# Kernel optimization log

Measured on AMD Instinct MI355X. Metric: run time of the kernel, lower is better.

## Reference

```python
import jax, jax.numpy as jnp
import numpy as np

EPS = 1e-6
DIAG_SIZE = 128  # triu band half-width (init kwarg diag_size)
NEG_INF = -1e9


def feature_map(x):
    # tanh feature map: phi(x) = tanh(x) + 1 (positive feature map)
    return jnp.tanh(x) + 1.0


def causal_dot_product(Q, K, V):
    # Q,K: [N,L,H,E], V: [N,L,H,D]
    # running KV state: S_l = sum_{s<=l} K_s V_s^T, materialized via cumsum
    kv = jnp.cumsum(jnp.einsum('nlhe,nlhd->nlhed', K, V), axis=1)  # [N,L,H,E,D]
    return jnp.einsum('nlhe,nlhed->nlhd', Q, kv)


def setup_inputs() -> dict:
    key = jax.random.key(0)
    k1, k2, k3 = jax.random.split(key, 3)
    N, L, H, E = 2, 2048, 8, 64
    queries = jax.random.normal(k1, (N, L, H, E), dtype=jnp.float32)
    keys = jax.random.normal(k2, (N, L, H, E), dtype=jnp.float32)
    values = jax.random.normal(k3, (N, L, H, E), dtype=jnp.float32)
    key_lengths_mask = jnp.ones((N, L), dtype=jnp.float32)  # all keys valid
    blend = jnp.full((1,), 0.9, dtype=jnp.float32)  # learned blend param (init 0.9)
    return {"queries": queries, "keys": keys, "values": values,
            "key_lengths_mask": key_lengths_mask, "blend": blend}


def reference(queries, keys, values, key_lengths_mask, blend):
    N, L, H, E = queries.shape
    # ---- linear attention path (kernel_1 = tanh, kernel_2 = 'none') ----
    Q1 = feature_map(queries)
    K1 = feature_map(keys) * key_lengths_mask[:, :, None, None]
    Z1 = 1.0 / (jnp.einsum('nlhi,nlhi->nlh', Q1, jnp.cumsum(K1, axis=1)) + EPS)
    LV = causal_dot_product(Q1, K1, values) * Z1[..., None]  # [N,L,H,D]
    # ---- full softmax attention path (banded by triu) ----
    softmax_temp = 1.0 / np.sqrt(E).astype(np.float32)
    QK = jnp.einsum('nlhe,nshe->nhls', queries, keys)  # [N,H,L,L]
    l_idx = jnp.arange(L)[:, None]
    s_idx = jnp.arange(L)[None, :]
    causal_add = jnp.where(s_idx <= l_idx, 0.0, NEG_INF)  # lower-triangular mask
    key_add = jnp.where(key_lengths_mask > 0, 0.0, NEG_INF)  # [N,L]
    logits = softmax_temp * (QK + causal_add[None, None] + key_add[:, None, None, :])
    A = jax.nn.softmax(logits, axis=-1)
    # torch.triu(A, diagonal=-diag_size): keep s >= l - diag_size
    band = s_idx >= (l_idx - DIAG_SIZE)
    A = jnp.where(band[None, None], A, 0.0)
    # dropout: eval mode (identity)
    SV = jnp.einsum('nhls,nshd->nlhd', A, values)
    b = blend[0]
    return b * SV + (1.0 - b) * LV
```

## Files before the change

### kernel.cpp

```cpp
#include <hip/hip_runtime.h>
#include <math.h>

#define N_ 2
#define L_ 2048
#define H_ 8
#define E_ 64
#define D_ 64
#define C_ 128
#define NC (L_/C_)
#define ROWSTRIDE (H_*E_)
#define TEMP 0.125f
#define EPS_F 1e-6f
#define NEG_INF_F (-1e9f)
#define CHUNK_WS (E_*D_ + E_)
#define NCHUNKS (N_*H_*NC)
#define TPAD 136
#define PPAD 72

typedef __attribute__((ext_vector_type(8))) short short8;
typedef __attribute__((ext_vector_type(4))) float f32x4;

__device__ __forceinline__ short f2bf(float x) {
  unsigned u = __float_as_uint(x);
  u += 0x7fffu + ((u >> 16) & 1u);
  return (short)(u >> 16);
}
__device__ __forceinline__ float bf2f(short s) {
  return __uint_as_float(((unsigned)(unsigned short)s) << 16);
}
__device__ __forceinline__ float tanh1f(float x) {
  float e = __expf(-2.f * x);
  return 2.f * __builtin_amdgcn_rcpf(1.f + e);
}

__device__ __forceinline__ void load_bf16_tile(short* __restrict__ dst,
                                               const float* __restrict__ src) {
  const int t = threadIdx.x;
#pragma unroll
  for (int it = 0; it < 4; ++it) {
    int gi = it * 256 + t;
    int row = gi >> 3, g = gi & 7;
    const float* p = src + row * ROWSTRIDE + g * 8;
    float4 a = *(const float4*)p;
    float4 b = *(const float4*)(p + 4);
    short8 v;
    v[0] = f2bf(a.x); v[1] = f2bf(a.y); v[2] = f2bf(a.z); v[3] = f2bf(a.w);
    v[4] = f2bf(b.x); v[5] = f2bf(b.y); v[6] = f2bf(b.z); v[7] = f2bf(b.w);
    int sg = g ^ (row & 7);
    *(short8*)(dst + row * 64 + sg * 8) = v;
  }
}

__device__ __forceinline__ short8 frag_ld(const short* __restrict__ buf,
                                          int rowbase, int hf, int lane) {
  int r = rowbase + (lane & 15);
  int g = (hf * 4 + (lane >> 4)) ^ (r & 7);
  return *(const short8*)(buf + r * 64 + g * 8);
}
__device__ __forceinline__ short8 frag_ldT(const short* __restrict__ buf,
                                           int nbase, int g, int lane) {
  int r = nbase + (lane & 15);
  return *(const short8*)(buf + r * TPAD + g * 8);
}
__device__ __forceinline__ short8 frag_ldP(const short* __restrict__ buf,
                                           int rowbase, int ks, int lane) {
  int r = rowbase + (lane & 15);
  int g = ks * 4 + (lane >> 4);
  return *(const short8*)(buf + r * PPAD + g * 8);
}

extern "C" __global__ void __launch_bounds__(256)
k_pre(const float* __restrict__ Q, const float* __restrict__ K,
      const float* __restrict__ V, const float* __restrict__ mask,
      float* __restrict__ ws, float* __restrict__ part) {
  __shared__ short ldsA[64 * TPAD];
  __shared__ short ldsB[64 * TPAD];
  __shared__ float fmsk[C_];
  const int orig = blockIdx.x;
  const int swz = (orig & 7) * 304 + (orig >> 3);
  const int t = threadIdx.x;
  const int w = t >> 6, lane = t & 63;
  const int col_lo = lane & 15;

  if (swz < 2176) {
    const int nh = swz / 136;
    const int p = swz - nh * 136;
    int qb = (int)((sqrtf(8.f * p + 1.f) - 1.f) * 0.5f);
    while ((qb + 1) * (qb + 2) / 2 <= p) ++qb;
    while (qb * (qb + 1) / 2 > p) --qb;
    const int kb = p - qb * (qb + 1) / 2;
    const int h = nh & (H_ - 1), n = nh >> 3;

    load_bf16_tile(ldsA, Q + ((n * L_ + qb * C_) * H_ + h) * E_);
    load_bf16_tile(ldsB, K + ((n * L_ + kb * C_) * H_ + h) * E_);
    if (t < C_) fmsk[t] = mask[n * L_ + kb * C_ + t];
    __syncthreads();

    const int rowbase = w * 32;
    short8 afr[2][2];
#pragma unroll
    for (int m = 0; m < 2; ++m)
#pragma unroll
      for (int hh = 0; hh < 2; ++hh)
        afr[m][hh] = frag_ld(ldsA, rowbase + 16 * m, hh, lane);

    f32x4 acc[2][8];
#pragma unroll
    for (int m = 0; m < 2; ++m)
#pragma unroll
      for (int c = 0; c < 8; ++c) acc[m][c] = (f32x4){0.f, 0.f, 0.f, 0.f};

#pragma unroll
    for (int c = 0; c < 8; ++c) {
      short8 b0 = frag_ld(ldsB, 16 * c, 0, lane);
      short8 b1 = frag_ld(ldsB, 16 * c, 1, lane);
#pragma unroll
      for (int m = 0; m < 2; ++m) {
        acc[m][c] = __builtin_amdgcn_mfma_f32_16x16x32_bf16(afr[m][0], b0, acc[m][c], 0, 0, 0);
        acc[m][c] = __builtin_amdgcn_mfma_f32_16x16x32_bf16(afr[m][1], b1, acc[m][c], 0, 0, 0);
      }
    }

    const bool diag = (kb == qb);
    float* pout = part + (size_t)(nh * NC + qb) * C_ * 16;
#pragma unroll
    for (int m = 0; m < 2; ++m) {
      const int rbase = rowbase + 16 * m + ((lane >> 4) << 2);
      float rs[4] = {0.f, 0.f, 0.f, 0.f};
#pragma unroll
      for (int c = 0; c < 8; ++c) {
        const int col = 16 * c + col_lo;
        const float madd = (fmsk[col] > 0.f) ? 0.f : NEG_INF_F;
#pragma unroll
        for (int reg = 0; reg < 4; ++reg) {
          float x = acc[m][c][reg] + madd;
          if (diag && col > rbase + reg) x += NEG_INF_F;
          rs[reg] += __expf(x * TEMP);
        }
      }
#pragma unroll
      for (int off = 1; off < 16; off <<= 1) {
#pragma unroll
        for (int reg = 0; reg < 4; ++reg) rs[reg] += __shfl_xor(rs[reg], off);
      }
      if (col_lo == 0) {
#pragma unroll
        for (int reg = 0; reg < 4; ++reg) pout[(rbase + reg) * 16 + kb] = rs[reg];
      }
    }
  } else {
    const int id = swz - 2176;
    const int nh = id >> 4, c = id & 15;
    const int h = nh & (H_ - 1), n = nh >> 3;
    const int gbase = ((n * L_ + c * C_) * H_ + h) * E_;
    const int e = t & 63, sb = t >> 6;
    const int mbase = n * L_ + c * C_;
#pragma unroll
    for (int q = 0; q < 4; ++q) {
      int s0 = sb * 32 + q * 8;
      short8 kk, vv;
#pragma unroll
      for (int j = 0; j < 8; ++j) {
        float kx = K[gbase + (s0 + j) * ROWSTRIDE + e];
        kk[j] = f2bf(tanh1f(kx) * mask[mbase + s0 + j]);
        vv[j] = f2bf(V[gbase + (s0 + j) * ROWSTRIDE + e]);
      }
      *(short8*)(ldsA + e * TPAD + (s0 >> 3) * 8) = kk;
      *(short8*)(ldsB + e * TPAD + (s0 >> 3) * 8) = vv;
    }
    __syncthreads();

    f32x4 acc[4];
#pragma unroll
    for (int nn = 0; nn < 4; ++nn) acc[nn] = (f32x4){0.f, 0.f, 0.f, 0.f};
#pragma unroll
    for (int ks = 0; ks < 4; ++ks) {
      short8 a = frag_ldT(ldsB, 16 * w, ks * 4 + (lane >> 4), lane);
#pragma unroll
      for (int nn = 0; nn < 4; ++nn) {
        short8 b = frag_ldT(ldsA, 16 * nn, ks * 4 + (lane >> 4), lane);
        acc[nn] = __builtin_amdgcn_mfma_f32_16x16x32_bf16(a, b, acc[nn], 0, 0, 0);
      }
    }
    float* wsc = ws + (size_t)(nh * NC + c) * CHUNK_WS;
    const int drow = 16 * w + ((lane >> 4) << 2);
#pragma unroll
    for (int nn = 0; nn < 4; ++nn)
#pragma unroll
      for (int reg = 0; reg < 4; ++reg)
        wsc[(16 * nn + col_lo) * D_ + drow + reg] = acc[nn][reg];
    if (t < 64) {
      float s = 0.f;
#pragma unroll
      for (int g = 0; g < 16; ++g) {
        short8 v = *(const short8*)(ldsA + t * TPAD + g * 8);
#pragma unroll
        for (int j = 0; j < 8; ++j) s += bf2f(v[j]);
      }
      wsc[E_ * D_ + t] = s;
    }
  }
}

extern "C" __global__ void __launch_bounds__(256)
k_scan(float* __restrict__ ws) {
  const int bid = blockIdx.x;
  const int swz = (bid & 7) * 34 + (bid >> 3);
  const int nh = swz / 17, seg = swz - nh * 17;
  const int idx = seg * 256 + threadIdx.x;
  if (idx >= CHUNK_WS) return;
  float* base = ws + (size_t)nh * NC * CHUNK_WS + idx;
  float v[NC];
#pragma unroll
  for (int c = 0; c < NC; ++c) v[c] = base[(size_t)c * CHUNK_WS];
  float acc = 0.f;
#pragma unroll
  for (int c = 0; c < NC; ++c) {
    base[(size_t)c * CHUNK_WS] = acc;
    acc += v[c];
  }
}

extern "C" __global__ void __launch_bounds__(256, 2)
k_fused(const float* __restrict__ Q, const float* __restrict__ K,
        const float* __restrict__ V, const float* __restrict__ mask,
        const float* __restrict__ blend, const float* __restrict__ ws,
        const float* __restrict__ part, float* __restrict__ out) {
  __shared__ short kbuf[C_ * 64];
  __shared__ short kv[64 * TPAD];
  __shared__ short pbuf[64 * PPAD];
  __shared__ float zlds[64];
  __shared__ float dinv[64];
  __shared__ float ksum[E_];
  __shared__ float kmC[C_];
  __shared__ float kmP[C_];

  const int orig = blockIdx.x;
  const int swz = (orig & 7) * 64 + (orig >> 3);
  const int rh = swz & 1, qb = (swz >> 1) & (NC - 1), nh = swz >> 5;
  const int h = nh & (H_ - 1), n = nh >> 3;
  const int t = threadIdx.x;
  const int w = t >> 6, lane = t & 63;
  const int rowbase = w * 16;
  const int col_lo = lane & 15;
  const int rb = rowbase + ((lane >> 4) << 2);
  const int rtile0 = rh * 64 + rb;
  const int qgbase = ((n * L_ + qb * C_ + rh * 64) * H_ + h) * E_;
  const int kbase_chunk = ((n * L_ + qb * C_) * H_ + h) * E_;
  const float* wsc = ws + (size_t)(nh * NC + qb) * CHUNK_WS;
  const float bl = blend[0];
  const float ob = 1.f - bl;
  const int d = t & 63, sb = t >> 6;
  const bool haveprev = (qb > 0);
  const int kgp = ((n * L_ + (qb - 1) * C_) * H_ + h) * E_;

  {
    const float* mrow = mask + n * L_ + qb * C_;
#pragma unroll
    for (int it = 0; it < 4; ++it) {
      int gi = it * 256 + t, row = gi >> 3, g = gi & 7;
      const float* p = K + kbase_chunk + row * ROWSTRIDE + g * 8;
      float4 a = *(const float4*)p, b = *(const float4*)(p + 4);
      float km = mrow[row];
      float xs[8] = {a.x, a.y, a.z, a.w, b.x, b.y, b.z, b.w};
      short8 v1;
#pragma unroll
      for (int j = 0; j < 8; ++j) v1[j] = f2bf(tanh1f(xs[j]) * km);
      *(short8*)(kbuf + row * 64 + (g ^ (row & 7)) * 8) = v1;
    }
  }
  {
    int eb = t >> 6;
#pragma unroll
    for (int q = 0; q < 2; ++q) {
      int e0 = eb * 16 + q * 8;
      short8 v;
#pragma unroll
      for (int j = 0; j < 8; ++j) v[j] = f2bf(wsc[(e0 + j) * D_ + d]);
      *(short8*)(kv + d * TPAD + (e0 >> 3) * 8) = v;
    }
  }
  if (t < 64) {
    ksum[t] = wsc[E_ * D_ + t];
    const float* pb = part + ((size_t)(nh * NC + qb) * C_ + rh * 64 + t) * 16;
    float4 a = *(const float4*)pb, b = *(const float4*)(pb + 4);
    float4 c = *(const float4*)(pb + 8), d4 = *(const float4*)(pb + 12);
    float vv[16] = {a.x, a.y, a.z, a.w, b.x, b.y, b.z, b.w,
                    c.x, c.y, c.z, c.w, d4.x, d4.y, d4.z, d4.w};
    float s = 0.f;
#pragma unroll
    for (int j = 0; j < 16; ++j) s += (j <= qb) ? vv[j] : 0.f;
    dinv[t] = 1.f / s;
  }
  if (t < C_) {
    kmC[t] = mask[n * L_ + qb * C_ + t];
    kmP[t] = haveprev ? mask[n * L_ + (qb - 1) * C_ + t] : 1.f;
  }
  __syncthreads();

  short8 af1[2];
  {
    const float* qp = Q + qgbase + (rowbase + (lane & 15)) * ROWSTRIDE;
#pragma unroll
    for (int kh = 0; kh < 2; ++kh) {
      int c0 = (kh * 4 + (lane >> 4)) * 8;
      float4 a = *(const float4*)(qp + c0);
      float4 b = *(const float4*)(qp + c0 + 4);
      float xs[8] = {a.x, a.y, a.z, a.w, b.x, b.y, b.z, b.w};
#pragma unroll
      for (int j = 0; j < 8; ++j) af1[kh][j] = f2bf(tanh1f(xs[j]));
    }
  }
  f32x4 c1[8];
#pragma unroll
  for (int ct = 0; ct < 8; ++ct) c1[ct] = (f32x4){0.f, 0.f, 0.f, 0.f};
#pragma unroll
  for (int ct = 0; ct < 8; ++ct) {
    short8 b0 = frag_ld(kbuf, 16 * ct, 0, lane);
    short8 b1 = frag_ld(kbuf, 16 * ct, 1, lane);
    c1[ct] = __builtin_amdgcn_mfma_f32_16x16x32_bf16(af1[0], b0, c1[ct], 0, 0, 0);
    c1[ct] = __builtin_amdgcn_mfma_f32_16x16x32_bf16(af1[1], b1, c1[ct], 0, 0, 0);
  }
  {
    float zz = 0.f;
#pragma unroll
    for (int kh = 0; kh < 2; ++kh) {
      int cb = (kh * 4 + (lane >> 4)) * 8;
#pragma unroll
      for (int j = 0; j < 8; ++j) zz += bf2f(af1[kh][j]) * ksum[cb + j];
    }
    zz += __shfl_xor(zz, 16);
    zz += __shfl_xor(zz, 32);
    if (lane < 16) zlds[rowbase + lane] = zz;
  }
  float rs[4] = {0.f, 0.f, 0.f, 0.f};
#pragma unroll
  for (int ct = 0; ct < 8; ++ct) {
    int col = 16 * ct + col_lo;
#pragma unroll
    for (int reg = 0; reg < 4; ++reg) {
      if (col <= rtile0 + reg) rs[reg] += c1[ct][reg];
      else c1[ct][reg] = 0.f;
    }
  }
#pragma unroll
  for (int off = 1; off < 16; off <<= 1)
#pragma unroll
    for (int reg = 0; reg < 4; ++reg) rs[reg] += __shfl_xor(rs[reg], off);

  f32x4 accO[4];
#pragma unroll
  for (int nn = 0; nn < 4; ++nn) accO[nn] = (f32x4){0.f, 0.f, 0.f, 0.f};
#pragma unroll
  for (int ks = 0; ks < 2; ++ks) {
    short8 bf[4];
#pragma unroll
    for (int nn = 0; nn < 4; ++nn)
      bf[nn] = frag_ldT(kv, 16 * nn, ks * 4 + (lane >> 4), lane);
#pragma unroll
    for (int nn = 0; nn < 4; ++nn)
      accO[nn] = __builtin_amdgcn_mfma_f32_16x16x32_bf16(af1[ks], bf[nn], accO[nn], 0, 0, 0);
  }
  float zrf[4], sdv[4];
#pragma unroll
  for (int reg = 0; reg < 4; ++reg) {
    zrf[reg] = ob / (zlds[rb + reg] + rs[reg] + EPS_F);
    sdv[reg] = bl * dinv[rb + reg];
  }
#pragma unroll
  for (int nn = 0; nn < 4; ++nn)
#pragma unroll
    for (int reg = 0; reg < 4; ++reg) accO[nn][reg] *= zrf[reg];
#pragma unroll
  for (int ct = 0; ct < 8; ++ct)
#pragma unroll
    for (int reg = 0; reg < 4; ++reg) c1[ct][reg] *= zrf[reg];
  __syncthreads();

#pragma unroll
  for (int it = 0; it < 4; ++it) {
    int gi = it * 256 + t, row = gi >> 3, g = gi & 7;
    const float* p = K + kbase_chunk + row * ROWSTRIDE + g * 8;
    float4 a = *(const float4*)p, b = *(const float4*)(p + 4);
    short8 v;
    v[0] = f2bf(a.x); v[1] = f2bf(a.y); v[2] = f2bf(a.z); v[3] = f2bf(a.w);
    v[4] = f2bf(b.x); v[5] = f2bf(b.y); v[6] = f2bf(b.z); v[7] = f2bf(b.w);
    *(short8*)(kbuf + row * 64 + (g ^ (row & 7)) * 8) = v;
  }
#pragma unroll
  for (int q = 0; q < 4; ++q) {
    int s0 = sb * 32 + q * 8;
    short8 v;
#pragma unroll
    for (int j = 0; j < 8; ++j) v[j] = f2bf(V[kbase_chunk + (s0 + j) * ROWSTRIDE + d]);
    *(short8*)(kv + d * TPAD + (s0 >> 3) * 8) = v;
  }
  __syncthreads();

#pragma unroll
  for (int hh = 0; hh < 2; ++hh) {
#pragma unroll
    for (int ch = 0; ch < 4; ++ch) {
      int ct = 4 * hh + ch, colh = 16 * ch + col_lo;
#pragma unroll
      for (int reg = 0; reg < 4; ++reg)
        pbuf[(rb + reg) * PPAD + colh] = f2bf(c1[ct][reg]);
    }
#pragma unroll
    for (int ks = 0; ks < 2; ++ks) {
      short8 ap = frag_ldP(pbuf, rowbase, ks, lane);
      short8 bv[4];
#pragma unroll
      for (int nn = 0; nn < 4; ++nn)
        bv[nn] = frag_ldT(kv, 16 * nn, 8 * hh + ks * 4 + (lane >> 4), lane);
#pragma unroll
      for (int nn = 0; nn < 4; ++nn)
        accO[nn] = __builtin_amdgcn_mfma_f32_16x16x32_bf16(ap, bv[nn], accO[nn], 0, 0, 0);
    }
  }

  {
    short8 afs[2];
    const float* qp = Q + qgbase + (rowbase + (lane & 15)) * ROWSTRIDE;
#pragma unroll
    for (int kh = 0; kh < 2; ++kh) {
      int c0 = (kh * 4 + (lane >> 4)) * 8;
      float4 a = *(const float4*)(qp + c0);
      float4 b = *(const float4*)(qp + c0 + 4);
      float xs[8] = {a.x, a.y, a.z, a.w, b.x, b.y, b.z, b.w};
#pragma unroll
      for (int j = 0; j < 8; ++j) afs[kh][j] = f2bf(xs[j]);
    }
#pragma unroll
    for (int ct = 0; ct < 8; ++ct) c1[ct] = (f32x4){0.f, 0.f, 0.f, 0.f};
#pragma unroll
    for (int ct = 0; ct < 8; ++ct) {
      short8 b0 = frag_ld(kbuf, 16 * ct, 0, lane);
      short8 b1 = frag_ld(kbuf, 16 * ct, 1, lane);
      c1[ct] = __builtin_amdgcn_mfma_f32_16x16x32_bf16(afs[0], b0, c1[ct], 0, 0, 0);
      c1[ct] = __builtin_amdgcn_mfma_f32_16x16x32_bf16(afs[1], b1, c1[ct], 0, 0, 0);
    }
#pragma unroll
    for (int ct = 0; ct < 8; ++ct) {
      int col = 16 * ct + col_lo;
      float madd = (kmC[col] > 0.f) ? 0.f : NEG_INF_F;
#pragma unroll
      for (int reg = 0; reg < 4; ++reg) {
        float x = c1[ct][reg] + madd;
        if (col > rtile0 + reg) x += NEG_INF_F;
        c1[ct][reg] = sdv[reg] * __expf(x * TEMP);
      }
    }
#pragma unroll
    for (int hh = 0; hh < 2; ++hh) {
#pragma unroll
      for (int ch = 0; ch < 4; ++ch) {
        int ct = 4 * hh + ch, colh = 16 * ch + col_lo;
#pragma unroll
        for (int reg = 0; reg < 4; ++reg)
          pbuf[(rb + reg) * PPAD + colh] = f2bf(c1[ct][reg]);
      }
#pragma unroll
      for (int ks = 0; ks < 2; ++ks) {
        short8 ap = frag_ldP(pbuf, rowbase, ks, lane);
        short8 bv[4];
#pragma unroll
        for (int nn = 0; nn < 4; ++nn)
          bv[nn] = frag_ldT(kv, 16 * nn, 8 * hh + ks * 4 + (lane >> 4), lane);
#pragma unroll
        for (int nn = 0; nn < 4; ++nn)
          accO[nn] = __builtin_amdgcn_mfma_f32_16x16x32_bf16(ap, bv[nn], accO[nn], 0, 0, 0);
      }
    }
  }

  if (haveprev) {
    __syncthreads();
#pragma unroll
    for (int it = 0; it < 4; ++it) {
      int gi = it * 256 + t, row = gi >> 3, g = gi & 7;
      const float* p = K + kgp + row * ROWSTRIDE + g * 8;
      float4 a = *(const float4*)p, b = *(const float4*)(p + 4);
      short8 v;
      v[0] = f2bf(a.x); v[1] = f2bf(a.y); v[2] = f2bf(a.z); v[3] = f2bf(a.w);
      v[4] = f2bf(b.x); v[5] = f2bf(b.y); v[6] = f2bf(b.z); v[7] = f2bf(b.w);
      *(short8*)(kbuf + row * 64 + (g ^ (row & 7)) * 8) = v;
    }
#pragma unroll
    for (int q = 0; q < 4; ++q) {
      int s0 = sb * 32 + q * 8;
      short8 v;
#pragma unroll
      for (int j = 0; j < 8; ++j) v[j] = f2bf(V[kgp + (s0 + j) * ROWSTRIDE + d]);
      *(short8*)(kv + d * TPAD + (s0 >> 3) * 8) = v;
    }
    __syncthreads();

    short8 afs[2];
    const float* qp = Q + qgbase + (rowbase + (lane & 15)) * ROWSTRIDE;
#pragma unroll
    for (int kh = 0; kh < 2; ++kh) {
      int c0 = (kh * 4 + (lane >> 4)) * 8;
      float4 a = *(const float4*)(qp + c0);
      float4 b = *(const float4*)(qp + c0 + 4);
      float xs[8] = {a.x, a.y, a.z, a.w, b.x, b.y, b.z, b.w};
#pragma unroll
      for (int j = 0; j < 8; ++j) afs[kh][j] = f2bf(xs[j]);
    }
#pragma unroll
    for (int ct = 0; ct < 8; ++ct) c1[ct] = (f32x4){0.f, 0.f, 0.f, 0.f};
#pragma unroll
    for (int ct = 0; ct < 8; ++ct) {
      short8 b0 = frag_ld(kbuf, 16 * ct, 0, lane);
      short8 b1 = frag_ld(kbuf, 16 * ct, 1, lane);
      c1[ct] = __builtin_amdgcn_mfma_f32_16x16x32_bf16(afs[0], b0, c1[ct], 0, 0, 0);
      c1[ct] = __builtin_amdgcn_mfma_f32_16x16x32_bf16(afs[1], b1, c1[ct], 0, 0, 0);
    }
#pragma unroll
    for (int ct = 0; ct < 8; ++ct) {
      int col = 16 * ct + col_lo;
      float madd = (kmP[col] > 0.f) ? 0.f : NEG_INF_F;
#pragma unroll
      for (int reg = 0; reg < 4; ++reg) {
        float x = c1[ct][reg] + madd;
        float pp = sdv[reg] * __expf(x * TEMP);
        if (col < rtile0 + reg) pp = 0.f;
        c1[ct][reg] = pp;
      }
    }
#pragma unroll
    for (int hh = 0; hh < 2; ++hh) {
#pragma unroll
      for (int ch = 0; ch < 4; ++ch) {
        int ct = 4 * hh + ch, colh = 16 * ch + col_lo;
#pragma unroll
        for (int reg = 0; reg < 4; ++reg)
          pbuf[(rb + reg) * PPAD + colh] = f2bf(c1[ct][reg]);
      }
#pragma unroll
      for (int ks = 0; ks < 2; ++ks) {
        short8 ap = frag_ldP(pbuf, rowbase, ks, lane);
        short8 bv[4];
#pragma unroll
        for (int nn = 0; nn < 4; ++nn)
          bv[nn] = frag_ldT(kv, 16 * nn, 8 * hh + ks * 4 + (lane >> 4), lane);
#pragma unroll
        for (int nn = 0; nn < 4; ++nn)
          accO[nn] = __builtin_amdgcn_mfma_f32_16x16x32_bf16(ap, bv[nn], accO[nn], 0, 0, 0);
      }
    }
  }

#pragma unroll
  for (int nn = 0; nn < 4; ++nn)
#pragma unroll
    for (int reg = 0; reg < 4; ++reg)
      out[qgbase + (rb + reg) * ROWSTRIDE + 16 * nn + col_lo] = accO[nn][reg];
}

extern "C" void kernel_launch(void* const* d_in, const int* in_sizes, int n_in,
                              void* d_out, int out_size, void* d_ws, size_t ws_size,
                              hipStream_t stream) {
  (void)in_sizes; (void)n_in; (void)out_size; (void)ws_size;
  const float* Q = (const float*)d_in[0];
  const float* K = (const float*)d_in[1];
  const float* V = (const float*)d_in[2];
  const float* mask = (const float*)d_in[3];
  const float* blend = (const float*)d_in[4];
  float* out = (float*)d_out;
  float* ws = (float*)d_ws;
  float* part = ws + (size_t)NCHUNKS * CHUNK_WS;

  k_pre<<<dim3(2432), dim3(256), 0, stream>>>(Q, K, V, mask, ws, part);
  k_scan<<<dim3(272), dim3(256), 0, stream>>>(ws);
  k_fused<<<dim3(N_ * H_ * NC * 2), dim3(256), 0, stream>>>(Q, K, V, mask, blend, ws, part, out);
}
```

Baseline: 48.17 us.

## Reuse band-tile exp scores from pre-pass instead of recomputing QK in fused kernel

The pre-pass, which already computes QK scores for every causal tile, now also writes unnormalized bf16 exp values for the diagonal and previous-diagonal tiles to workspace. The fused kernel reads these probability tiles directly instead of reloading K, recomputing QK with MFMA and redoing the exp. Row normalisation is applied once at the end through a separate accumulator. This trades recompute for extra global writes and reads, about 2 x 32 KB per chunk, and adds write traffic to the pre-pass.

```diff
diff --git a/kernel.cpp b/kernel.cpp
--- a/kernel.cpp
+++ b/kernel.cpp
@@ -33,8 +33,9 @@
   return 2.f * __builtin_amdgcn_rcpf(1.f + e);
 }
 
-__device__ __forceinline__ void load_bf16_tile(short* __restrict__ dst,
-                                               const float* __restrict__ src) {
+template <typename F>
+__device__ __forceinline__ void stage_tile(short* __restrict__ dst,
+                                           const float* __restrict__ src, F f) {
   const int t = threadIdx.x;
 #pragma unroll
   for (int it = 0; it < 4; ++it) {
@@ -43,11 +44,11 @@
     const float* p = src + row * ROWSTRIDE + g * 8;
     float4 a = *(const float4*)p;
     float4 b = *(const float4*)(p + 4);
+    float xs[8] = {a.x, a.y, a.z, a.w, b.x, b.y, b.z, b.w};
     short8 v;
-    v[0] = f2bf(a.x); v[1] = f2bf(a.y); v[2] = f2bf(a.z); v[3] = f2bf(a.w);
-    v[4] = f2bf(b.x); v[5] = f2bf(b.y); v[6] = f2bf(b.z); v[7] = f2bf(b.w);
-    int sg = g ^ (row & 7);
-    *(short8*)(dst + row * 64 + sg * 8) = v;
+#pragma unroll
+    for (int j = 0; j < 8; ++j) v[j] = f2bf(f(xs[j], row));
+    *(short8*)(dst + row * 64 + (g ^ (row & 7)) * 8) = v;
   }
 }
 
@@ -72,7 +73,8 @@
 extern "C" __global__ void __launch_bounds__(256)
 k_pre(const float* __restrict__ Q, const float* __restrict__ K,
       const float* __restrict__ V, const float* __restrict__ mask,
-      float* __restrict__ ws, float* __restrict__ part) {
+      float* __restrict__ ws, float* __restrict__ part,
+      short* __restrict__ pd, short* __restrict__ pp) {
   __shared__ short ldsA[64 * TPAD];
   __shared__ short ldsB[64 * TPAD];
   __shared__ float fmsk[C_];
@@ -91,8 +93,10 @@
     const int kb = p - qb * (qb + 1) / 2;
     const int h = nh & (H_ - 1), n = nh >> 3;
 
-    load_bf16_tile(ldsA, Q + ((n * L_ + qb * C_) * H_ + h) * E_);
-    load_bf16_tile(ldsB, K + ((n * L_ + kb * C_) * H_ + h) * E_);
+    stage_tile(ldsA, Q + ((n * L_ + qb * C_) * H_ + h) * E_,
+               [](float x, int) { return x; });
+    stage_tile(ldsB, K + ((n * L_ + kb * C_) * H_ + h) * E_,
+               [](float x, int) { return x; });
     if (t < C_) fmsk[t] = mask[n * L_ + kb * C_ + t];
     __syncthreads();
 
@@ -122,6 +126,9 @@
     }
 
     const bool diag = (kb == qb);
+    const bool prev = (kb == qb - 1);
+    const bool band = diag || prev;
+    short* pt = (diag ? pd : pp) + (size_t)(nh * NC + qb) * (C_ * C_);
     float* pout = part + (size_t)(nh * NC + qb) * C_ * 16;
 #pragma unroll
     for (int m = 0; m < 2; ++m) {
@@ -135,7 +142,12 @@
         for (int reg = 0; reg < 4; ++reg) {
           float x = acc[m][c][reg] + madd;
           if (diag && col > rbase + reg) x += NEG_INF_F;
-          rs[reg] += __expf(x * TEMP);
+          float e = __expf(x * TEMP);
+          rs[reg] += e;
+          if (band) {
+            if (prev && col < rbase + reg) e = 0.f;
+            pt[(rbase + reg) * C_ + col] = f2bf(e);
+          }
         }
       }
 #pragma unroll
@@ -225,15 +237,14 @@
 k_fused(const float* __restrict__ Q, const float* __restrict__ K,
         const float* __restrict__ V, const float* __restrict__ mask,
         const float* __restrict__ blend, const float* __restrict__ ws,
-        const float* __restrict__ part, float* __restrict__ out) {
+        const float* __restrict__ part, const short* __restrict__ pd,
+        const short* __restrict__ pp, float* __restrict__ out) {
   __shared__ short kbuf[C_ * 64];
   __shared__ short kv[64 * TPAD];
   __shared__ short pbuf[64 * PPAD];
   __shared__ float zlds[64];
   __shared__ float dinv[64];
   __shared__ float ksum[E_];
-  __shared__ float kmC[C_];
-  __shared__ float kmP[C_];
 
   const int orig = blockIdx.x;
   const int swz = (orig & 7) * 64 + (orig >> 3);
@@ -292,10 +303,6 @@
     for (int j = 0; j < 16; ++j) s += (j <= qb) ? vv[j] : 0.f;
     dinv[t] = 1.f / s;
   }
-  if (t < C_) {
-    kmC[t] = mask[n * L_ + qb * C_ + t];
-    kmP[t] = haveprev ? mask[n * L_ + (qb - 1) * C_ + t] : 1.f;
-  }
   __syncthreads();
 
   short8 af1[2];
@@ -378,16 +385,6 @@
   __syncthreads();
 
 #pragma unroll
-  for (int it = 0; it < 4; ++it) {
-    int gi = it * 256 + t, row = gi >> 3, g = gi & 7;
-    const float* p = K + kbase_chunk + row * ROWSTRIDE + g * 8;
-    float4 a = *(const float4*)p, b = *(const float4*)(p + 4);
-    short8 v;
-    v[0] = f2bf(a.x); v[1] = f2bf(a.y); v[2] = f2bf(a.z); v[3] = f2bf(a.w);
-    v[4] = f2bf(b.x); v[5] = f2bf(b.y); v[6] = f2bf(b.z); v[7] = f2bf(b.w);
-    *(short8*)(kbuf + row * 64 + (g ^ (row & 7)) * 8) = v;
-  }
-#pragma unroll
   for (int q = 0; q < 4; ++q) {
     int s0 = sb * 32 + q * 8;
     short8 v;
@@ -400,8 +397,8 @@
 #pragma unroll
   for (int hh = 0; hh < 2; ++hh) {
 #pragma unroll
-    for (int ch = 0; ch < 4; ++ch) {
-      int ct = 4 * hh + ch, colh = 16 * ch + col_lo;
+    for (int cc = 0; cc < 4; ++cc) {
+      int ct = 4 * hh + cc, colh = 16 * cc + col_lo;
 #pragma unroll
       for (int reg = 0; reg < 4; ++reg)
         pbuf[(rb + reg) * PPAD + colh] = f2bf(c1[ct][reg]);
@@ -419,46 +416,19 @@
     }
   }
 
+  f32x4 accS[4];
+#pragma unroll
+  for (int nn = 0; nn < 4; ++nn) accS[nn] = (f32x4){0.f, 0.f, 0.f, 0.f};
   {
-    short8 afs[2];
-    const float* qp = Q + qgbase + (rowbase + (lane & 15)) * ROWSTRIDE;
-#pragma unroll
-    for (int kh = 0; kh < 2; ++kh) {
-      int c0 = (kh * 4 + (lane >> 4)) * 8;
-      float4 a = *(const float4*)(qp + c0);
-      float4 b = *(const float4*)(qp + c0 + 4);
-      float xs[8] = {a.x, a.y, a.z, a.w, b.x, b.y, b.z, b.w};
-#pragma unroll
-      for (int j = 0; j < 8; ++j) afs[kh][j] = f2bf(xs[j]);
-    }
-#pragma unroll
-    for (int ct = 0; ct < 8; ++ct) c1[ct] = (f32x4){0.f, 0.f, 0.f, 0.f};
-#pragma unroll
-    for (int ct = 0; ct < 8; ++ct) {
-      short8 b0 = frag_ld(kbuf, 16 * ct, 0, lane);
-      short8 b1 = frag_ld(kbuf, 16 * ct, 1, lane);
-      c1[ct] = __builtin_amdgcn_mfma_f32_16x16x32_bf16(afs[0], b0, c1[ct], 0, 0, 0);
-      c1[ct] = __builtin_amdgcn_mfma_f32_16x16x32_bf16(afs[1], b1, c1[ct], 0, 0, 0);
-    }
-#pragma unroll
-    for (int ct = 0; ct < 8; ++ct) {
-      int col = 16 * ct + col_lo;
-      float madd = (kmC[col] > 0.f) ? 0.f : NEG_INF_F;
-#pragma unroll
-      for (int reg = 0; reg < 4; ++reg) {
-        float x = c1[ct][reg] + madd;
-        if (col > rtile0 + reg) x += NEG_INF_F;
-        c1[ct][reg] = sdv[reg] * __expf(x * TEMP);
-      }
-    }
+    const short* ps = pd + (size_t)(nh * NC + qb) * (C_ * C_) + (size_t)(rh * 64) * C_;
 #pragma unroll
     for (int hh = 0; hh < 2; ++hh) {
 #pragma unroll
-      for (int ch = 0; ch < 4; ++ch) {
-        int ct = 4 * hh + ch, colh = 16 * ch + col_lo;
-#pragma unroll
-        for (int reg = 0; reg < 4; ++reg)
-          pbuf[(rb + reg) * PPAD + colh] = f2bf(c1[ct][reg]);
+      for (int i = 0; i < 2; ++i) {
+        int idx = i * 64 + lane;
+        int rl = rowbase + (idx >> 3), g = idx & 7;
+        short8 v = *(const short8*)(ps + (size_t)rl * C_ + 64 * hh + g * 8);
+        *(short8*)(pbuf + rl * PPAD + g * 8) = v;
       }
 #pragma unroll
       for (int ks = 0; ks < 2; ++ks) {
@@ -469,23 +439,13 @@
           bv[nn] = frag_ldT(kv, 16 * nn, 8 * hh + ks * 4 + (lane >> 4), lane);
 #pragma unroll
         for (int nn = 0; nn < 4; ++nn)
-          accO[nn] = __builtin_amdgcn_mfma_f32_16x16x32_bf16(ap, bv[nn], accO[nn], 0, 0, 0);
+          accS[nn] = __builtin_amdgcn_mfma_f32_16x16x32_bf16(ap, bv[nn], accS[nn], 0, 0, 0);
       }
     }
   }
 
   if (haveprev) {
     __syncthreads();
-#pragma unroll
-    for (int it = 0; it < 4; ++it) {
-      int gi = it * 256 + t, row = gi >> 3, g = gi & 7;
-      const float* p = K + kgp + row * ROWSTRIDE + g * 8;
-      float4 a = *(const float4*)p, b = *(const float4*)(p + 4);
-      short8 v;
-      v[0] = f2bf(a.x); v[1] = f2bf(a.y); v[2] = f2bf(a.z); v[3] = f2bf(a.w);
-      v[4] = f2bf(b.x); v[5] = f2bf(b.y); v[6] = f2bf(b.z); v[7] = f2bf(b.w);
-      *(short8*)(kbuf + row * 64 + (g ^ (row & 7)) * 8) = v;
-    }
 #pragma unroll
     for (int q = 0; q < 4; ++q) {
       int s0 = sb * 32 + q * 8;
@@ -496,46 +456,15 @@
     }
     __syncthreads();
 
-    short8 afs[2];
-    const float* qp = Q + qgbase + (rowbase + (lane & 15)) * ROWSTRIDE;
-#pragma unroll
-    for (int kh = 0; kh < 2; ++kh) {
-      int c0 = (kh * 4 + (lane >> 4)) * 8;
-      float4 a = *(const float4*)(qp + c0);
-      float4 b = *(const float4*)(qp + c0 + 4);
-      float xs[8] = {a.x, a.y, a.z, a.w, b.x, b.y, b.z, b.w};
-#pragma unroll
-      for (int j = 0; j < 8; ++j) afs[kh][j] = f2bf(xs[j]);
-    }
-#pragma unroll
-    for (int ct = 0; ct < 8; ++ct) c1[ct] = (f32x4){0.f, 0.f, 0.f, 0.f};
-#pragma unroll
-    for (int ct = 0; ct < 8; ++ct) {
-      short8 b0 = frag_ld(kbuf, 16 * ct, 0, lane);
-      short8 b1 = frag_ld(kbuf, 16 * ct, 1, lane);
-      c1[ct] = __builtin_amdgcn_mfma_f32_16x16x32_bf16(afs[0], b0, c1[ct], 0, 0, 0);
-      c1[ct] = __builtin_amdgcn_mfma_f32_16x16x32_bf16(afs[1], b1, c1[ct], 0, 0, 0);
-    }
-#pragma unroll
-    for (int ct = 0; ct < 8; ++ct) {
-      int col = 16 * ct + col_lo;
-      float madd = (kmP[col] > 0.f) ? 0.f : NEG_INF_F;
-#pragma unroll
-      for (int reg = 0; reg < 4; ++reg) {
-        float x = c1[ct][reg] + madd;
-        float pp = sdv[reg] * __expf(x * TEMP);
-        if (col < rtile0 + reg) pp = 0.f;
-        c1[ct][reg] = pp;
-      }
-    }
+    const short* ps = pp + (size_t)(nh * NC + qb) * (C_ * C_) + (size_t)(rh * 64) * C_;
 #pragma unroll
     for (int hh = 0; hh < 2; ++hh) {
 #pragma unroll
-      for (int ch = 0; ch < 4; ++ch) {
-        int ct = 4 * hh + ch, colh = 16 * ch + col_lo;
-#pragma unroll
-        for (int reg = 0; reg < 4; ++reg)
-          pbuf[(rb + reg) * PPAD + colh] = f2bf(c1[ct][reg]);
+      for (int i = 0; i < 2; ++i) {
+        int idx = i * 64 + lane;
+        int rl = rowbase + (idx >> 3), g = idx & 7;
+        short8 v = *(const short8*)(ps + (size_t)rl * C_ + 64 * hh + g * 8);
+        *(short8*)(pbuf + rl * PPAD + g * 8) = v;
       }
 #pragma unroll
       for (int ks = 0; ks < 2; ++ks) {
@@ -546,7 +475,7 @@
           bv[nn] = frag_ldT(kv, 16 * nn, 8 * hh + ks * 4 + (lane >> 4), lane);
 #pragma unroll
         for (int nn = 0; nn < 4; ++nn)
-          accO[nn] = __builtin_amdgcn_mfma_f32_16x16x32_bf16(ap, bv[nn], accO[nn], 0, 0, 0);
+          accS[nn] = __builtin_amdgcn_mfma_f32_16x16x32_bf16(ap, bv[nn], accS[nn], 0, 0, 0);
       }
     }
   }
@@ -555,7 +484,8 @@
   for (int nn = 0; nn < 4; ++nn)
 #pragma unroll
     for (int reg = 0; reg < 4; ++reg)
-      out[qgbase + (rb + reg) * ROWSTRIDE + 16 * nn + col_lo] = accO[nn][reg];
+      out[qgbase + (rb + reg) * ROWSTRIDE + 16 * nn + col_lo] =
+          accO[nn][reg] + sdv[reg] * accS[nn][reg];
 }
 
 extern "C" void kernel_launch(void* const* d_in, const int* in_sizes, int n_in,
@@ -570,8 +500,10 @@
   float* out = (float*)d_out;
   float* ws = (float*)d_ws;
   float* part = ws + (size_t)NCHUNKS * CHUNK_WS;
-
-  k_pre<<<dim3(2432), dim3(256), 0, stream>>>(Q, K, V, mask, ws, part);
+  short* pd = (short*)(part + (size_t)NCHUNKS * C_ * 16);
+  short* pp = pd + (size_t)NCHUNKS * C_ * C_;
+
+  k_pre<<<dim3(2432), dim3(256), 0, stream>>>(Q, K, V, mask, ws, part, pd, pp);
   k_scan<<<dim3(272), dim3(256), 0, stream>>>(ws);
-  k_fused<<<dim3(N_ * H_ * NC * 2), dim3(256), 0, stream>>>(Q, K, V, mask, blend, ws, part, out);
-}
+  k_fused<<<dim3(N_ * H_ * NC * 2), dim3(256), 0, stream>>>(Q, K, V, mask, blend, ws, part, pd, pp, out);
+}
```

After: 46.02 us (median of 2 runs). 4.5% less time.
